# Kernel optimization log

Measured on AMD Instinct MI355X. Metric: run time of the kernel, lower is better.

## Reference

```python
import jax, jax.numpy as jnp
import numpy as np

N_NODES = 50000
N_EDGES = 600000
FEAT = 256
HID = 128
LAYERS = 3
CLASSES = 32


def setup_inputs() -> dict:
    key = jax.random.key(0)
    ks = jax.random.split(key, 10)
    s = 0.05
    return {
        "object_features": jax.random.normal(ks[0], (N_NODES, FEAT), jnp.float32),
        "edge_index": jax.random.randint(ks[1], (2, N_EDGES), 0, N_NODES, jnp.int64),
        "emb_w": jax.random.normal(ks[2], (FEAT, HID), jnp.float32) * s,
        "emb_b": jnp.zeros((HID,), jnp.float32),
        "rel_w": jax.random.normal(ks[3], (LAYERS, HID, HID), jnp.float32) * s,
        "rel_b": jnp.zeros((LAYERS, HID), jnp.float32),
        "root_w": jax.random.normal(ks[4], (LAYERS, HID, HID), jnp.float32) * s,
        "head_w": jax.random.normal(ks[5], (2 * HID, CLASSES), jnp.float32) * s,
        "head_b": jnp.zeros((CLASSES,), jnp.float32),
    }


def reference(object_features, edge_index, emb_w, emb_b, rel_w, rel_b, root_w, head_w, head_b):
    n = object_features.shape[0]
    src, dst = edge_index[0], edge_index[1]
    # node embedding + relu
    x = jax.nn.relu(object_features @ emb_w + emb_b)  # [N, H]
    # stacked GraphConv layers: x' = relu(W_rel @ sum_{j->i} x_j + b + W_root @ x)
    for i in range(rel_w.shape[0]):
        agg = jax.ops.segment_sum(x[src], dst, num_segments=n)  # scatter-add messages
        x = jax.nn.relu(agg @ rel_w[i] + rel_b[i] + x @ root_w[i])
    # edge head: gather endpoints, concat, linear
    edge_feat = jnp.concatenate([x[src], x[dst]], axis=-1)  # [E, 2H]
    return edge_feat @ head_w + head_b  # [E, C]
```

## Files before the change

### kernel.cpp

```cpp
#include <hip/hip_runtime.h>
#include <hip/hip_bf16.h>

#define FEAT 256
#define HID 128
#define CLASSES 32
#define LAYERS 3

typedef float f4 __attribute__((ext_vector_type(4)));
typedef float f2 __attribute__((ext_vector_type(2)));
typedef __attribute__((ext_vector_type(8))) short short8;
typedef __attribute__((ext_vector_type(4))) float f32x4;
typedef unsigned int u32;
typedef __attribute__((ext_vector_type(4))) unsigned int u32x4;

__device__ __forceinline__ unsigned short bf16_rne(float v) {
    unsigned u = __float_as_uint(v);
    return (unsigned short)((u + 0x7FFF + ((u >> 16) & 1)) >> 16);
}
__device__ __forceinline__ u32 bf16x2_rne(float a, float b) {
    return (u32)bf16_rne(a) | ((u32)bf16_rne(b) << 16);
}


__global__ void count_kernel(const int* __restrict__ dst, int* __restrict__ counts, int E) {
    int e = blockIdx.x * blockDim.x + threadIdx.x;
    if (e < E) atomicAdd(&counts[dst[e]], 1);
}

__global__ void partial_kernel(const int* __restrict__ counts, int* __restrict__ partials, int N) {
    int t = threadIdx.x;
    int i = blockIdx.x * 256 + t;
    int v = (i < N) ? counts[i] : 0;
#pragma unroll
    for (int off = 32; off >= 1; off >>= 1) v += __shfl_down(v, off, 64);
    __shared__ int ws[4];
    if ((t & 63) == 0) ws[t >> 6] = v;
    __syncthreads();
    if (t == 0) partials[blockIdx.x] = ws[0] + ws[1] + ws[2] + ws[3];
}

__global__ void scan_partials_kernel(const int* __restrict__ partials, int* __restrict__ poff, int NB) {
    int t = threadIdx.x, lane = t & 63, w = t >> 6;
    int v = (t < NB) ? partials[t] : 0;
    int x = v;
#pragma unroll
    for (int off = 1; off < 64; off <<= 1) {
        int y = __shfl_up(x, off, 64);
        if (lane >= off) x += y;
    }
    __shared__ int ws[4];
    if (lane == 63) ws[w] = x;
    __syncthreads();
    int woff = 0;
    for (int k = 0; k < w; ++k) woff += ws[k];
    if (t < NB) poff[t] = woff + x - v;
}

__global__ void scan_final_kernel(const int* __restrict__ counts, const int* __restrict__ poff,
                                  int* __restrict__ row_off, int* __restrict__ cursor, int N) {
    int t = threadIdx.x, lane = t & 63, w = t >> 6;
    int i = blockIdx.x * 256 + t;
    int v = (i < N) ? counts[i] : 0;
    int x = v;
#pragma unroll
    for (int off = 1; off < 64; off <<= 1) {
        int y = __shfl_up(x, off, 64);
        if (lane >= off) x += y;
    }
    __shared__ int ws[4];
    if (lane == 63) ws[w] = x;
    __syncthreads();
    int woff = 0;
    for (int k = 0; k < w; ++k) woff += ws[k];
    int excl = poff[blockIdx.x] + woff + x - v;
    if (i < N) {
        row_off[i] = excl;
        cursor[i] = excl;
        if (i == N - 1) row_off[N] = excl + v;
    }
}

__global__ void fill_kernel(const int* __restrict__ src, const int* __restrict__ dst,
                            int* __restrict__ cursor, int* __restrict__ csr_src, int E) {
    int e = blockIdx.x * blockDim.x + threadIdx.x;
    if (e < E) {
        int pos = atomicAdd(&cursor[dst[e]], 1);
        csr_src[pos] = src[e];
    }
}

__global__ void prep_kernel(const float* __restrict__ emb_w, const float* __restrict__ rel_w,
                            const float* __restrict__ root_w, const float* __restrict__ head_w,
                            unsigned short* __restrict__ we, unsigned short* __restrict__ wl,
                            unsigned short* __restrict__ wp) {
    int idx = blockIdx.x * 256 + threadIdx.x;
    if (idx < 128 * 256) {
        int n = idx >> 8, k = idx & 255;
        we[n * 256 + k] = bf16_rne(emb_w[k * 128 + n]);
    } else if (idx < 4 * 128 * 256) {
        int i = idx - 128 * 256;
        int l = i >> 15;
        int r = i & 32767;
        int n = r >> 8, k = r & 255;
        float v = (k < 128) ? rel_w[l * 16384 + k * 128 + n] : root_w[l * 16384 + (k - 128) * 128 + n];
        wl[i] = bf16_rne(v);
    } else if (idx < 4 * 128 * 256 + 64 * 128) {
        int i = idx - 4 * 128 * 256;
        int c = i >> 7, k = i & 127;
        float v = (c < 32) ? head_w[k * 32 + c] : head_w[(128 + k) * 32 + (c - 32)];
        wp[c * 128 + k] = bf16_rne(v);
    }
}

template <int NCOL, int KTOT, bool RELU, int AFMT, bool PACKOUT>
__global__ __launch_bounds__(256) void gemm_mfma(
    const void* __restrict__ A0v, int lda0,
    const void* __restrict__ A1v, int lda1, int K0,
    const unsigned short* __restrict__ W,
    const float* __restrict__ bias, void* __restrict__ outv, int M) {
    constexpr int NCHUNK = KTOT / 32;
    constexpr int WCOL = NCOL / 4;
    constexpr int NCT = WCOL / 16;

    int wv = threadIdx.x >> 6;
    int lane = threadIdx.x & 63;
    int m16 = lane & 15;
    int quad = lane >> 4;
    int colbase = wv * WCOL;
    int rowblk = blockIdx.x * 64;

    short8 Bf[NCT][NCHUNK];
#pragma unroll
    for (int ct = 0; ct < NCT; ++ct)
#pragma unroll
        for (int kc = 0; kc < NCHUNK; ++kc)
            Bf[ct][kc] = *(const short8*)(const void*)(W + (size_t)(colbase + ct * 16 + m16) * KTOT + kc * 32 + quad * 8);

    float bcol[NCT];
#pragma unroll
    for (int ct = 0; ct < NCT; ++ct) bcol[ct] = bias ? bias[colbase + ct * 16 + m16] : 0.f;

    f32x4 acc[4][NCT] = {};

    auto aaddr = [&](int t, int kc) -> const void* {
        int r = rowblk + t * 16 + m16;
        r = (r < M) ? r : (M - 1);
        bool second = (kc * 32 >= K0);
        int lda = second ? lda1 : lda0;
        int kofs = kc * 32 - (second ? K0 : 0);
        if (AFMT == 0)
            return (const float*)(second ? A1v : A0v) + (size_t)r * lda + kofs + quad * 8;
        else
            return (const unsigned short*)(second ? A1v : A0v) + (size_t)r * lda + kofs + quad * 8;
    };

    if (AFMT == 1) {
        short8 Ac[NCHUNK], An[NCHUNK];
#pragma unroll
        for (int kc = 0; kc < NCHUNK; ++kc) Ac[kc] = *(const short8*)aaddr(0, kc);
#pragma unroll
        for (int t = 0; t < 4; ++t) {
            if (t + 1 < 4) {
#pragma unroll
                for (int kc = 0; kc < NCHUNK; ++kc) An[kc] = *(const short8*)aaddr(t + 1, kc);
            }
#pragma unroll
            for (int kc = 0; kc < NCHUNK; ++kc)
#pragma unroll
                for (int ct = 0; ct < NCT; ++ct)
                    acc[t][ct] = __builtin_amdgcn_mfma_f32_16x16x32_bf16(Ac[kc], Bf[ct][kc], acc[t][ct], 0, 0, 0);
            if (t + 1 < 4) {
#pragma unroll
                for (int kc = 0; kc < NCHUNK; ++kc) Ac[kc] = An[kc];
            }
        }
    } else {
#pragma unroll
        for (int t = 0; t < 4; ++t) {
            u32x4 raw[NCHUNK][2];
#pragma unroll
            for (int kc = 0; kc < NCHUNK; ++kc) {
                const u32x4* p = (const u32x4*)aaddr(t, kc);
                raw[kc][0] = p[0];
                raw[kc][1] = p[1];
            }
#pragma unroll
            for (int kc = 0; kc < NCHUNK; ++kc) {
                union { u32x4 u[2]; float f[8]; } cv;
                cv.u[0] = raw[kc][0];
                cv.u[1] = raw[kc][1];
                short8 Af;
#pragma unroll
                for (int j = 0; j < 8; ++j) Af[j] = (short)bf16_rne(cv.f[j]);
#pragma unroll
                for (int ct = 0; ct < NCT; ++ct)
                    acc[t][ct] = __builtin_amdgcn_mfma_f32_16x16x32_bf16(Af, Bf[ct][kc], acc[t][ct], 0, 0, 0);
            }
        }
    }

#pragma unroll
    for (int t = 0; t < 4; ++t) {
#pragma unroll
        for (int r = 0; r < 4; ++r) {
            int row = rowblk + t * 16 + quad * 4 + r;
            if (row < M) {
#pragma unroll
                for (int ct = 0; ct < NCT; ++ct) {
                    float v = acc[t][ct][r] + bcol[ct];
                    if (RELU) v = fmaxf(v, 0.f);
                    size_t idx = (size_t)row * NCOL + colbase + ct * 16 + m16;
                    if (PACKOUT) ((unsigned short*)outv)[idx] = bf16_rne(v);
                    else ((float*)outv)[idx] = v;
                }
            }
        }
    }
}

__global__ void aggregate_kernel(const u32* __restrict__ x, const int* __restrict__ row_off,
                                 const int* __restrict__ csr, u32* __restrict__ agg, int N) {
    int gw = (blockIdx.x * 256 + threadIdx.x) >> 6;
    int lane = threadIdx.x & 63;
    if (gw >= N) return;
    int beg = row_off[gw], end = row_off[gw + 1];

    f2 a0 = (f2)0.f, a1 = (f2)0.f, a2 = (f2)0.f, a3 = (f2)0.f;

    auto unp = [](u32 u) -> f2 {
        f2 r;
        r[0] = __uint_as_float(u << 16);
        r[1] = __uint_as_float(u & 0xFFFF0000u);
        return r;
    };

    int nfull = (end - beg) >> 2;
    int j = beg;
    if (nfull > 0) {
        int s0 = csr[j], s1 = csr[j + 1], s2 = csr[j + 2], s3 = csr[j + 3];
        for (int b = 1; b < nfull; ++b) {
            u32 v0 = x[(size_t)s0 * 64 + lane];
            u32 v1 = x[(size_t)s1 * 64 + lane];
            u32 v2 = x[(size_t)s2 * 64 + lane];
            u32 v3 = x[(size_t)s3 * 64 + lane];
            int jn = j + 4;
            s0 = csr[jn]; s1 = csr[jn + 1]; s2 = csr[jn + 2]; s3 = csr[jn + 3];
            a0 += unp(v0); a1 += unp(v1); a2 += unp(v2); a3 += unp(v3);
            j = jn;
        }
        u32 v0 = x[(size_t)s0 * 64 + lane];
        u32 v1 = x[(size_t)s1 * 64 + lane];
        u32 v2 = x[(size_t)s2 * 64 + lane];
        u32 v3 = x[(size_t)s3 * 64 + lane];
        a0 += unp(v0); a1 += unp(v1); a2 += unp(v2); a3 += unp(v3);
        j += 4;
    }

    int rem = end - j;
    if (rem > 0) {
        int e1 = end - 1;
        int t0 = csr[j];
        int t1 = csr[min(j + 1, e1)];
        int t2 = csr[min(j + 2, e1)];
        u32 w0 = x[(size_t)t0 * 64 + lane];
        u32 w1 = x[(size_t)t1 * 64 + lane];
        u32 w2 = x[(size_t)t2 * 64 + lane];
        a0 += unp(w0);
        if (rem > 1) a1 += unp(w1);
        if (rem > 2) a2 += unp(w2);
    }

    f2 a = (a0 + a2) + (a1 + a3);
    agg[(size_t)gw * 64 + lane] = bf16x2_rne(a[0], a[1]);
}

__global__ void edge_out_kernel(const int* __restrict__ src, const int* __restrict__ dst,
                                const float* __restrict__ pspd, const float* __restrict__ head_b,
                                float* __restrict__ out, int E) {
    int idx = blockIdx.x * blockDim.x + threadIdx.x;
    int e = idx >> 3;
    int c4 = (idx & 7) * 4;
    if (e >= E) return;
    int s = src[e], d = dst[e];
    f4 a = *(const f4*)&pspd[(size_t)s * 64 + c4];
    f4 b = *(const f4*)&pspd[(size_t)d * 64 + 32 + c4];
    f4 hb = *(const f4*)&head_b[c4];
    f4 o = a + b + hb;
    *(f4*)&out[(size_t)e * CLASSES + c4] = o;
}


extern "C" void kernel_launch(void* const* d_in, const int* in_sizes, int n_in,
                              void* d_out, int out_size, void* d_ws, size_t ws_size,
                              hipStream_t stream) {
    const float* feat   = (const float*)d_in[0];
    const int*   eidx   = (const int*)d_in[1];
    const float* emb_w  = (const float*)d_in[2];
    const float* emb_b  = (const float*)d_in[3];
    const float* rel_w  = (const float*)d_in[4];
    const float* rel_b  = (const float*)d_in[5];
    const float* root_w = (const float*)d_in[6];
    const float* head_w = (const float*)d_in[7];
    const float* head_b = (const float*)d_in[8];
    float* out = (float*)d_out;

    int N = in_sizes[0] / FEAT;
    int E = in_sizes[1] / 2;
    const int* src = eidx;
    const int* dst = eidx + E;

    u32* xA  = (u32*)d_ws;
    u32* xB  = xA + (size_t)N * 64;
    u32* agg = xB + (size_t)N * 64;
    int* counts   = (int*)(agg + (size_t)N * 64);
    int* row_off  = counts + N;
    int* cursor   = row_off + (N + 1);
    int* csr_src  = cursor + N;
    int* partials = csr_src + E;
    int* poff     = partials + 256;
    int* iend     = poff + 256;
    size_t ioff = (size_t)(iend - (int*)d_ws);
    ioff = (ioff + 3) & ~(size_t)3;
    unsigned short* we = (unsigned short*)((int*)d_ws + ioff);
    unsigned short* wl = we + 128 * 256;
    unsigned short* wp = wl + 3 * 128 * 256;

    int NB = (N + 255) / 256;

    hipMemsetAsync(counts, 0, (size_t)N * sizeof(int), stream);
    count_kernel<<<(E + 255) / 256, 256, 0, stream>>>(dst, counts, E);
    partial_kernel<<<NB, 256, 0, stream>>>(counts, partials, N);
    scan_partials_kernel<<<1, 256, 0, stream>>>(partials, poff, NB);
    scan_final_kernel<<<NB, 256, 0, stream>>>(counts, poff, row_off, cursor, N);
    fill_kernel<<<(E + 255) / 256, 256, 0, stream>>>(src, dst, cursor, csr_src, E);

    prep_kernel<<<(4 * 128 * 256 + 64 * 128 + 255) / 256, 256, 0, stream>>>(
        emb_w, rel_w, root_w, head_w, we, wl, wp);

    int grid = (N + 63) / 64;
    gemm_mfma<HID, FEAT, true, 0, true><<<grid, 256, 0, stream>>>(
        feat, FEAT, nullptr, 0, FEAT, we, emb_b, xA, N);

    const u32* xin = xA;
    u32* xout = xB;
    for (int l = 0; l < LAYERS; ++l) {
        aggregate_kernel<<<(N * 64 + 255) / 256, 256, 0, stream>>>(xin, row_off, csr_src, agg, N);
        gemm_mfma<HID, 2 * HID, true, 1, true><<<grid, 256, 0, stream>>>(
            agg, HID, xin, HID, HID,
            wl + (size_t)l * 128 * 256, rel_b + (size_t)l * HID, xout, N);
        u32* tmp = (u32*)xin; xin = xout; xout = tmp;
    }

    float* pspd = (float*)agg;
    gemm_mfma<64, HID, false, 1, false><<<grid, 256, 0, stream>>>(
        xin, HID, nullptr, 0, HID, wp, nullptr, pspd, N);

    edge_out_kernel<<<((size_t)E * 8 + 255) / 256, 256, 0, stream>>>(src, dst, pspd, head_b, out, E);
}
```

Baseline: 414.2 us.

## Split GEMM columns across grid, pre-convert features to bf16, widen aggregation unroll

The MFMA GEMM now gives each wave one 16-column tile, with column blocks spread over a second grid dimension. This raises block count and cuts per-thread register use, at the cost of re-reading A rows once per column block. A separate kernel converts the fp32 input features to bf16 first, so the embedding GEMM loads bf16 directly; this adds an extra pass over the feature matrix and more workspace. The aggregation kernel now keeps 8 gathers in flight per iteration with an early exit for empty rows, aiming for more memory parallelism per wave.

```diff
diff --git a/kernel.cpp b/kernel.cpp
--- a/kernel.cpp
+++ b/kernel.cpp
@@ -112,91 +112,59 @@
     }
 }
 
-template <int NCOL, int KTOT, bool RELU, int AFMT, bool PACKOUT>
-__global__ __launch_bounds__(256) void gemm_mfma(
-    const void* __restrict__ A0v, int lda0,
-    const void* __restrict__ A1v, int lda1, int K0,
+__global__ void cvt_feat_kernel(const float* __restrict__ f, unsigned short* __restrict__ o, int n8) {
+    int i = blockIdx.x * 256 + threadIdx.x;
+    if (i >= n8) return;
+    f4 a = *(const f4*)(f + (size_t)i * 8);
+    f4 b = *(const f4*)(f + (size_t)i * 8 + 4);
+    short8 s;
+    s[0] = (short)bf16_rne(a[0]); s[1] = (short)bf16_rne(a[1]);
+    s[2] = (short)bf16_rne(a[2]); s[3] = (short)bf16_rne(a[3]);
+    s[4] = (short)bf16_rne(b[0]); s[5] = (short)bf16_rne(b[1]);
+    s[6] = (short)bf16_rne(b[2]); s[7] = (short)bf16_rne(b[3]);
+    *(short8*)(o + (size_t)i * 8) = s;
+}
+
+template <int NCOL, int KTOT, bool RELU, bool PACKOUT>
+__global__ __launch_bounds__(256) void gemm_reg(
+    const unsigned short* __restrict__ A0, int lda0,
+    const unsigned short* __restrict__ A1, int lda1, int K0,
     const unsigned short* __restrict__ W,
     const float* __restrict__ bias, void* __restrict__ outv, int M) {
     constexpr int NCHUNK = KTOT / 32;
-    constexpr int WCOL = NCOL / 4;
-    constexpr int NCT = WCOL / 16;
 
     int wv = threadIdx.x >> 6;
     int lane = threadIdx.x & 63;
     int m16 = lane & 15;
     int quad = lane >> 4;
-    int colbase = wv * WCOL;
+    int colbase = blockIdx.y * 64 + wv * 16;
     int rowblk = blockIdx.x * 64;
 
-    short8 Bf[NCT][NCHUNK];
-#pragma unroll
-    for (int ct = 0; ct < NCT; ++ct)
-#pragma unroll
-        for (int kc = 0; kc < NCHUNK; ++kc)
-            Bf[ct][kc] = *(const short8*)(const void*)(W + (size_t)(colbase + ct * 16 + m16) * KTOT + kc * 32 + quad * 8);
-
-    float bcol[NCT];
-#pragma unroll
-    for (int ct = 0; ct < NCT; ++ct) bcol[ct] = bias ? bias[colbase + ct * 16 + m16] : 0.f;
-
-    f32x4 acc[4][NCT] = {};
-
-    auto aaddr = [&](int t, int kc) -> const void* {
+    short8 Bf[NCHUNK];
+#pragma unroll
+    for (int kc = 0; kc < NCHUNK; ++kc)
+        Bf[kc] = *(const short8*)(const void*)(W + (size_t)(colbase + m16) * KTOT + kc * 32 + quad * 8);
+
+    float bcol = bias ? bias[colbase + m16] : 0.f;
+
+    f32x4 acc[4] = {};
+
+#pragma unroll
+    for (int t = 0; t < 4; ++t) {
         int r = rowblk + t * 16 + m16;
         r = (r < M) ? r : (M - 1);
-        bool second = (kc * 32 >= K0);
-        int lda = second ? lda1 : lda0;
-        int kofs = kc * 32 - (second ? K0 : 0);
-        if (AFMT == 0)
-            return (const float*)(second ? A1v : A0v) + (size_t)r * lda + kofs + quad * 8;
-        else
-            return (const unsigned short*)(second ? A1v : A0v) + (size_t)r * lda + kofs + quad * 8;
-    };
-
-    if (AFMT == 1) {
-        short8 Ac[NCHUNK], An[NCHUNK];
-#pragma unroll
-        for (int kc = 0; kc < NCHUNK; ++kc) Ac[kc] = *(const short8*)aaddr(0, kc);
-#pragma unroll
-        for (int t = 0; t < 4; ++t) {
-            if (t + 1 < 4) {
-#pragma unroll
-                for (int kc = 0; kc < NCHUNK; ++kc) An[kc] = *(const short8*)aaddr(t + 1, kc);
-            }
-#pragma unroll
-            for (int kc = 0; kc < NCHUNK; ++kc)
-#pragma unroll
-                for (int ct = 0; ct < NCT; ++ct)
-                    acc[t][ct] = __builtin_amdgcn_mfma_f32_16x16x32_bf16(Ac[kc], Bf[ct][kc], acc[t][ct], 0, 0, 0);
-            if (t + 1 < 4) {
-#pragma unroll
-                for (int kc = 0; kc < NCHUNK; ++kc) Ac[kc] = An[kc];
-            }
+        short8 Af[NCHUNK];
+#pragma unroll
+        for (int kc = 0; kc < NCHUNK; ++kc) {
+            bool second = (kc * 32 >= K0);
+            const unsigned short* Ab = second ? A1 : A0;
+            int lda = second ? lda1 : lda0;
+            int kofs = kc * 32 - (second ? K0 : 0);
+            Af[kc] = *(const short8*)(const void*)(Ab + (size_t)r * lda + kofs + quad * 8);
         }
-    } else {
-#pragma unroll
-        for (int t = 0; t < 4; ++t) {
-            u32x4 raw[NCHUNK][2];
-#pragma unroll
-            for (int kc = 0; kc < NCHUNK; ++kc) {
-                const u32x4* p = (const u32x4*)aaddr(t, kc);
-                raw[kc][0] = p[0];
-                raw[kc][1] = p[1];
-            }
-#pragma unroll
-            for (int kc = 0; kc < NCHUNK; ++kc) {
-                union { u32x4 u[2]; float f[8]; } cv;
-                cv.u[0] = raw[kc][0];
-                cv.u[1] = raw[kc][1];
-                short8 Af;
-#pragma unroll
-                for (int j = 0; j < 8; ++j) Af[j] = (short)bf16_rne(cv.f[j]);
-#pragma unroll
-                for (int ct = 0; ct < NCT; ++ct)
-                    acc[t][ct] = __builtin_amdgcn_mfma_f32_16x16x32_bf16(Af, Bf[ct][kc], acc[t][ct], 0, 0, 0);
-            }
-        }
+#pragma unroll
+        for (int kc = 0; kc < NCHUNK; ++kc)
+            acc[t] = __builtin_amdgcn_mfma_f32_16x16x32_bf16(Af[kc], Bf[kc], acc[t], 0, 0, 0);
     }
 
 #pragma unroll
@@ -205,14 +173,11 @@
         for (int r = 0; r < 4; ++r) {
             int row = rowblk + t * 16 + quad * 4 + r;
             if (row < M) {
-#pragma unroll
-                for (int ct = 0; ct < NCT; ++ct) {
-                    float v = acc[t][ct][r] + bcol[ct];
-                    if (RELU) v = fmaxf(v, 0.f);
-                    size_t idx = (size_t)row * NCOL + colbase + ct * 16 + m16;
-                    if (PACKOUT) ((unsigned short*)outv)[idx] = bf16_rne(v);
-                    else ((float*)outv)[idx] = v;
-                }
+                float v = acc[t][r] + bcol;
+                if (RELU) v = fmaxf(v, 0.f);
+                size_t idx = (size_t)row * NCOL + colbase + m16;
+                if (PACKOUT) ((unsigned short*)outv)[idx] = bf16_rne(v);
+                else ((float*)outv)[idx] = v;
             }
         }
     }
@@ -225,7 +190,10 @@
     if (gw >= N) return;
     int beg = row_off[gw], end = row_off[gw + 1];
 
-    f2 a0 = (f2)0.f, a1 = (f2)0.f, a2 = (f2)0.f, a3 = (f2)0.f;
+    if (end <= beg) {
+        agg[(size_t)gw * 64 + lane] = 0u;
+        return;
+    }
 
     auto unp = [](u32 u) -> f2 {
         f2 r;
@@ -234,44 +202,36 @@
         return r;
     };
 
-    int nfull = (end - beg) >> 2;
+    f2 a[8];
+#pragma unroll
+    for (int k = 0; k < 8; ++k) a[k] = (f2)0.f;
+
+    int e1 = end - 1;
+    int s[8];
+#pragma unroll
+    for (int k = 0; k < 8; ++k) s[k] = csr[min(beg + k, e1)];
+
     int j = beg;
-    if (nfull > 0) {
-        int s0 = csr[j], s1 = csr[j + 1], s2 = csr[j + 2], s3 = csr[j + 3];
-        for (int b = 1; b < nfull; ++b) {
-            u32 v0 = x[(size_t)s0 * 64 + lane];
-            u32 v1 = x[(size_t)s1 * 64 + lane];
-            u32 v2 = x[(size_t)s2 * 64 + lane];
-            u32 v3 = x[(size_t)s3 * 64 + lane];
-            int jn = j + 4;
-            s0 = csr[jn]; s1 = csr[jn + 1]; s2 = csr[jn + 2]; s3 = csr[jn + 3];
-            a0 += unp(v0); a1 += unp(v1); a2 += unp(v2); a3 += unp(v3);
-            j = jn;
+    while (j < end) {
+        u32 v[8];
+#pragma unroll
+        for (int k = 0; k < 8; ++k) v[k] = x[(size_t)s[k] * 64 + lane];
+
+        int jn = j + 8;
+        if (jn < end) {
+#pragma unroll
+            for (int k = 0; k < 8; ++k) s[k] = csr[min(jn + k, e1)];
         }
-        u32 v0 = x[(size_t)s0 * 64 + lane];
-        u32 v1 = x[(size_t)s1 * 64 + lane];
-        u32 v2 = x[(size_t)s2 * 64 + lane];
-        u32 v3 = x[(size_t)s3 * 64 + lane];
-        a0 += unp(v0); a1 += unp(v1); a2 += unp(v2); a3 += unp(v3);
-        j += 4;
-    }
-
-    int rem = end - j;
-    if (rem > 0) {
-        int e1 = end - 1;
-        int t0 = csr[j];
-        int t1 = csr[min(j + 1, e1)];
-        int t2 = csr[min(j + 2, e1)];
-        u32 w0 = x[(size_t)t0 * 64 + lane];
-        u32 w1 = x[(size_t)t1 * 64 + lane];
-        u32 w2 = x[(size_t)t2 * 64 + lane];
-        a0 += unp(w0);
-        if (rem > 1) a1 += unp(w1);
-        if (rem > 2) a2 += unp(w2);
-    }
-
-    f2 a = (a0 + a2) + (a1 + a3);
-    agg[(size_t)gw * 64 + lane] = bf16x2_rne(a[0], a[1]);
+
+#pragma unroll
+        for (int k = 0; k < 8; ++k)
+            if (j + k < end) a[k] += unp(v[k]);
+
+        j = jn;
+    }
+
+    f2 r = ((a[0] + a[4]) + (a[1] + a[5])) + ((a[2] + a[6]) + (a[3] + a[7]));
+    agg[(size_t)gw * 64 + lane] = bf16x2_rne(r[0], r[1]);
 }
 
 __global__ void edge_out_kernel(const int* __restrict__ src, const int* __restrict__ dst,
@@ -309,10 +269,11 @@
     const int* src = eidx;
     const int* dst = eidx + E;
 
-    u32* xA  = (u32*)d_ws;
-    u32* xB  = xA + (size_t)N * 64;
-    u32* agg = xB + (size_t)N * 64;
-    int* counts   = (int*)(agg + (size_t)N * 64);
+    u32* xA    = (u32*)d_ws;
+    u32* xB    = xA + (size_t)N * 64;
+    u32* agg   = xB + (size_t)N * 64;
+    u32* featb = agg + (size_t)N * 64;
+    int* counts   = (int*)(featb + (size_t)N * 128);
     int* row_off  = counts + N;
     int* cursor   = row_off + (N + 1);
     int* csr_src  = cursor + N;
@@ -336,24 +297,25 @@
 
     prep_kernel<<<(4 * 128 * 256 + 64 * 128 + 255) / 256, 256, 0, stream>>>(
         emb_w, rel_w, root_w, head_w, we, wl, wp);
-
-    int grid = (N + 63) / 64;
-    gemm_mfma<HID, FEAT, true, 0, true><<<grid, 256, 0, stream>>>(
-        feat, FEAT, nullptr, 0, FEAT, we, emb_b, xA, N);
+    cvt_feat_kernel<<<(N * 32 + 255) / 256, 256, 0, stream>>>(feat, (unsigned short*)featb, N * 32);
+
+    int gm = (N + 63) / 64;
+    gemm_reg<HID, FEAT, true, true><<<dim3(gm, HID / 64), 256, 0, stream>>>(
+        (const unsigned short*)featb, FEAT, nullptr, 0, FEAT, we, emb_b, xA, N);
 
     const u32* xin = xA;
     u32* xout = xB;
     for (int l = 0; l < LAYERS; ++l) {
         aggregate_kernel<<<(N * 64 + 255) / 256, 256, 0, stream>>>(xin, row_off, csr_src, agg, N);
-        gemm_mfma<HID, 2 * HID, true, 1, true><<<grid, 256, 0, stream>>>(
-            agg, HID, xin, HID, HID,
+        gemm_reg<HID, 2 * HID, true, true><<<dim3(gm, HID / 64), 256, 0, stream>>>(
+            (const unsigned short*)agg, HID, (const unsigned short*)xin, HID, HID,
             wl + (size_t)l * 128 * 256, rel_b + (size_t)l * HID, xout, N);
         u32* tmp = (u32*)xin; xin = xout; xout = tmp;
     }
 
     float* pspd = (float*)agg;
-    gemm_mfma<64, HID, false, 1, false><<<grid, 256, 0, stream>>>(
-        xin, HID, nullptr, 0, HID, wp, nullptr, pspd, N);
+    gemm_reg<64, HID, false, false><<<dim3(gm, 1), 256, 0, stream>>>(
+        (const unsigned short*)xin, HID, nullptr, 0, HID, wp, nullptr, pspd, N);
 
     edge_out_kernel<<<((size_t)E * 8 + 255) / 256, 256, 0, stream>>>(src, dst, pspd, head_b, out, E);
 }
```

New measurement: 446.9 us. 7.9% more time.
